# Kernel tuning notes

Hardware: AMD Instinct MI355X
Metric: run time of the kernel (lower is better)

## Reference

```python
import jax, jax.numpy as jnp
import numpy as np

# NF4 codebook (bitsandbytes values)
NF4_LEVELS = jnp.array([-1.0, -0.6961928009986877, -0.5250730514526367, -0.39491748809814453,
                        -0.28444138169288635, -0.18477343022823334, -0.09105003625154495, 0.0,
                        0.07958029955625534, 0.16093020141124725, 0.24611230194568634,
                        0.33791524171829224, 0.44070982933044434, 0.5626170039176941,
                        0.7229568362236023, 1.0], dtype=jnp.float32)

IN_FEATURES = 4096
OUT_FEATURES = 4096


def setup_inputs() -> dict:
    key = jax.random.key(0)
    k1, k2, k3, k4 = jax.random.split(key, 4)
    x = jax.random.normal(k1, (4, 2048, IN_FEATURES), dtype=jnp.float32)
    # packed uint8 bytes (stored as int32 in [0,256)), shape (O, I//2)
    packed = jax.random.randint(k2, (OUT_FEATURES, IN_FEATURES // 2), 0, 256, dtype=jnp.int32)
    absmax = jax.random.uniform(k3, (OUT_FEATURES,), dtype=jnp.float32) + 1e-3
    bias = jax.random.normal(k4, (OUT_FEATURES,), dtype=jnp.float32)
    return {"x": x, "packed": packed, "absmax": absmax, "bias": bias}


def dequantize_nf4(packed, absmax):
    # packed: (O, I//2) int bytes; high nibble first, then low nibble
    high = (packed >> 4) & 15
    low = packed & 15
    idx = jnp.stack([high, low], axis=2).reshape(packed.shape[0], -1)  # (O, I)
    w = NF4_LEVELS[idx]                    # LUT dequant, (O, I)
    return w * absmax[:, None]             # per-row absmax scaling


def reference(x, packed, absmax, bias):
    # forward: dequantize weight on-the-fly, then F.linear(x, W, bias)
    w = dequantize_nf4(packed, absmax)     # (O, I)
    return jnp.einsum('bsi,oi->bso', x, w) + bias
```

## Files before the change

### kernel.cpp

```cpp
#include <hip/hip_runtime.h>
#include <hip/hip_bf16.h>
#include <stdint.h>

#define M_DIM 8192
#define N_DIM 4096
#define K_DIM 4096

typedef __bf16 bf16_t;
typedef __attribute__((ext_vector_type(8))) __bf16 bf16x8;
typedef __attribute__((ext_vector_type(4))) float f32x4;

__constant__ float NF4_LUT[16] = {
    -1.0f, -0.6961928009986877f, -0.5250730514526367f, -0.39491748809814453f,
    -0.28444138169288635f, -0.18477343022823334f, -0.09105003625154495f, 0.0f,
    0.07958029955625534f, 0.16093020141124725f, 0.24611230194568634f,
    0.33791524171829224f, 0.44070982933044434f, 0.5626170039176941f,
    0.7229568362236023f, 1.0f};

__global__ __launch_bounds__(256) void dequant_nf4_kernel(
    const int* __restrict__ packed, const float* __restrict__ absmax,
    bf16_t* __restrict__ W) {
  const int t = blockIdx.x * 256 + threadIdx.x;
  const int row = t >> 9;
  const int c = t & 511;
  const int4 p = ((const int4*)packed)[t];
  const float am = absmax[row];
  bf16x8 v;
  int bytes0 = p.x & 255, bytes1 = p.y & 255, bytes2 = p.z & 255, bytes3 = p.w & 255;
  v[0] = (bf16_t)(NF4_LUT[(bytes0 >> 4) & 15] * am);
  v[1] = (bf16_t)(NF4_LUT[bytes0 & 15] * am);
  v[2] = (bf16_t)(NF4_LUT[(bytes1 >> 4) & 15] * am);
  v[3] = (bf16_t)(NF4_LUT[bytes1 & 15] * am);
  v[4] = (bf16_t)(NF4_LUT[(bytes2 >> 4) & 15] * am);
  v[5] = (bf16_t)(NF4_LUT[bytes2 & 15] * am);
  v[6] = (bf16_t)(NF4_LUT[(bytes3 >> 4) & 15] * am);
  v[7] = (bf16_t)(NF4_LUT[bytes3 & 15] * am);
  *((bf16x8*)&W[(size_t)row * K_DIM + c * 8]) = v;
}

__global__ __launch_bounds__(256) void cvt_bf16_kernel(
    const float* __restrict__ x, bf16_t* __restrict__ y) {
  const int t = blockIdx.x * 256 + threadIdx.x;
  const float4 a = ((const float4*)x)[2 * t];
  const float4 b = ((const float4*)x)[2 * t + 1];
  bf16x8 v;
  v[0] = (bf16_t)a.x; v[1] = (bf16_t)a.y; v[2] = (bf16_t)a.z; v[3] = (bf16_t)a.w;
  v[4] = (bf16_t)b.x; v[5] = (bf16_t)b.y; v[6] = (bf16_t)b.z; v[7] = (bf16_t)b.w;
  *((bf16x8*)&y[(size_t)t * 8]) = v;
}

#define GLD_LDS16(g, l)                                                     \
  __builtin_amdgcn_global_load_lds(                                        \
      (const __attribute__((address_space(1))) void*)(g),                   \
      (__attribute__((address_space(3))) void*)(l), 16, 0, 0)

__global__ __launch_bounds__(256) void gemm_nf4_kernel(
    const bf16_t* __restrict__ A, const bf16_t* __restrict__ B,
    const float* __restrict__ bias, float* __restrict__ C) {
  constexpr int BM = 128, BN = 128, BK = 32;
  __shared__ __align__(16) bf16_t sA[BM * BK];
  __shared__ __align__(16) bf16_t sB[BN * BK];

  const int tid = threadIdx.x;
  const int wave = tid >> 6, lane = tid & 63;
  const int wr = wave >> 1, wc = wave & 1;
  const int quad = lane >> 4, l15 = lane & 15;

  const int blockM = blockIdx.y * BM;
  const int blockN = blockIdx.x * BN;

  const int sr = tid >> 2;
  const int sk = (tid & 3) * 8;
  const bf16_t* gA0 = A + (size_t)(blockM + sr) * K_DIM + sk;
  const bf16_t* gA1 = gA0 + (size_t)64 * K_DIM;
  const bf16_t* gB0 = B + (size_t)(blockN + sr) * K_DIM + sk;
  const bf16_t* gB1 = gB0 + (size_t)64 * K_DIM;
  bf16_t* lA0 = &sA[tid * 8];
  bf16_t* lA1 = &sA[tid * 8 + 64 * BK];
  bf16_t* lB0 = &sB[tid * 8];
  bf16_t* lB1 = &sB[tid * 8 + 64 * BK];

  f32x4 acc[4][4];
#pragma unroll
  for (int i = 0; i < 4; ++i)
#pragma unroll
    for (int j = 0; j < 4; ++j) acc[i][j] = (f32x4)(0.0f);

  for (int k0 = 0; k0 < K_DIM; k0 += BK) {
    GLD_LDS16(gA0 + k0, lA0);
    GLD_LDS16(gA1 + k0, lA1);
    GLD_LDS16(gB0 + k0, lB0);
    GLD_LDS16(gB1 + k0, lB1);
    __syncthreads();

    bf16x8 af[4], bfr[4];
#pragma unroll
    for (int i = 0; i < 4; ++i)
      af[i] = *(const bf16x8*)&sA[(wr * 64 + i * 16 + l15) * BK + quad * 8];
#pragma unroll
    for (int j = 0; j < 4; ++j)
      bfr[j] = *(const bf16x8*)&sB[(wc * 64 + j * 16 + l15) * BK + quad * 8];

#pragma unroll
    for (int i = 0; i < 4; ++i)
#pragma unroll
      for (int j = 0; j < 4; ++j)
        acc[i][j] = __builtin_amdgcn_mfma_f32_16x16x32_bf16(af[i], bfr[j],
                                                            acc[i][j], 0, 0, 0);
    __syncthreads();
  }

#pragma unroll
  for (int j = 0; j < 4; ++j) {
    const int n = blockN + wc * 64 + j * 16 + l15;
    const float bv = bias[n];
#pragma unroll
    for (int i = 0; i < 4; ++i) {
      const int m0 = blockM + wr * 64 + i * 16 + quad * 4;
      f32x4 v = acc[i][j];
      C[(size_t)(m0 + 0) * N_DIM + n] = v[0] + bv;
      C[(size_t)(m0 + 1) * N_DIM + n] = v[1] + bv;
      C[(size_t)(m0 + 2) * N_DIM + n] = v[2] + bv;
      C[(size_t)(m0 + 3) * N_DIM + n] = v[3] + bv;
    }
  }
}

__global__ __launch_bounds__(256) void fallback_kernel(
    const float* __restrict__ x, const int* __restrict__ packed,
    const float* __restrict__ absmax, const float* __restrict__ bias,
    float* __restrict__ out) {
  const int idx = blockIdx.x * 256 + threadIdx.x;
  const int m = idx / N_DIM, n = idx % N_DIM;
  const int* prow = packed + (size_t)n * (K_DIM / 2);
  const float* xr = x + (size_t)m * K_DIM;
  float s = 0.0f;
  for (int p = 0; p < K_DIM / 2; ++p) {
    const int b = prow[p] & 255;
    s += xr[2 * p] * NF4_LUT[(b >> 4) & 15] + xr[2 * p + 1] * NF4_LUT[b & 15];
  }
  out[idx] = s * absmax[n] + bias[n];
}

extern "C" void kernel_launch(void* const* d_in, const int* in_sizes, int n_in,
                              void* d_out, int out_size, void* d_ws,
                              size_t ws_size, hipStream_t stream) {
  const float* x = (const float*)d_in[0];
  const int* packed = (const int*)d_in[1];
  const float* absmax = (const float*)d_in[2];
  const float* bias = (const float*)d_in[3];
  float* out = (float*)d_out;

  const size_t wBytes = (size_t)N_DIM * K_DIM * sizeof(bf16_t);
  const size_t xBytes = (size_t)M_DIM * K_DIM * sizeof(bf16_t);
  if (ws_size < wBytes + xBytes) {
    fallback_kernel<<<dim3((M_DIM * N_DIM) / 256), dim3(256), 0, stream>>>(
        x, packed, absmax, bias, out);
    return;
  }

  bf16_t* W = (bf16_t*)d_ws;
  bf16_t* xb = (bf16_t*)((char*)d_ws + wBytes);

  dequant_nf4_kernel<<<dim3((N_DIM * (K_DIM / 2) / 4) / 256), dim3(256), 0,
                       stream>>>(packed, absmax, W);
  cvt_bf16_kernel<<<dim3((M_DIM * K_DIM / 8) / 256), dim3(256), 0, stream>>>(
      x, xb);
  gemm_nf4_kernel<<<dim3(N_DIM / 128, M_DIM / 128), dim3(256), 0, stream>>>(
      xb, W, bias, out);
}
```

Measured before the change: 545.8 us.

## Use conflict-free LDS layout in GEMM, bpermute LUT dequant, narrower cvt

Changes the GEMM's LDS staging layout so each 16-row by 32-k fragment sits contiguously in lane order. Fragment reads then become linear per-lane 16-byte loads instead of row-strided loads that conflict on LDS banks. The dequant kernel replaces constant-memory LUT lookups with ds_bpermute against a per-lane copy of the LUT held in registers. The conversion kernel moves to 4 elements per thread with more blocks. The cvt change may reduce memory efficiency slightly because each thread now issues smaller stores.

Result: slower. 712.4 us (+30.5%).

```diff
diff --git a/kernel.cpp b/kernel.cpp
--- a/kernel.cpp
+++ b/kernel.cpp
@@ -8,6 +8,7 @@
 
 typedef __bf16 bf16_t;
 typedef __attribute__((ext_vector_type(8))) __bf16 bf16x8;
+typedef __attribute__((ext_vector_type(4))) __bf16 bf16x4;
 typedef __attribute__((ext_vector_type(4))) float f32x4;
 
 __constant__ float NF4_LUT[16] = {
@@ -23,30 +24,32 @@
   const int t = blockIdx.x * 256 + threadIdx.x;
   const int row = t >> 9;
   const int c = t & 511;
+  const int lane = threadIdx.x & 63;
+  const int lutbits = __float_as_int(NF4_LUT[lane & 15]);
+
   const int4 p = ((const int4*)packed)[t];
   const float am = absmax[row];
   bf16x8 v;
-  int bytes0 = p.x & 255, bytes1 = p.y & 255, bytes2 = p.z & 255, bytes3 = p.w & 255;
-  v[0] = (bf16_t)(NF4_LUT[(bytes0 >> 4) & 15] * am);
-  v[1] = (bf16_t)(NF4_LUT[bytes0 & 15] * am);
-  v[2] = (bf16_t)(NF4_LUT[(bytes1 >> 4) & 15] * am);
-  v[3] = (bf16_t)(NF4_LUT[bytes1 & 15] * am);
-  v[4] = (bf16_t)(NF4_LUT[(bytes2 >> 4) & 15] * am);
-  v[5] = (bf16_t)(NF4_LUT[bytes2 & 15] * am);
-  v[6] = (bf16_t)(NF4_LUT[(bytes3 >> 4) & 15] * am);
-  v[7] = (bf16_t)(NF4_LUT[bytes3 & 15] * am);
+#pragma unroll
+  for (int q = 0; q < 4; ++q) {
+    const int byte = (q == 0 ? p.x : q == 1 ? p.y : q == 2 ? p.z : p.w) & 255;
+    const float hi =
+        __int_as_float(__builtin_amdgcn_ds_bpermute(((byte >> 4) & 15) << 2, lutbits));
+    const float lo =
+        __int_as_float(__builtin_amdgcn_ds_bpermute((byte & 15) << 2, lutbits));
+    v[2 * q] = (bf16_t)(hi * am);
+    v[2 * q + 1] = (bf16_t)(lo * am);
+  }
   *((bf16x8*)&W[(size_t)row * K_DIM + c * 8]) = v;
 }
 
 __global__ __launch_bounds__(256) void cvt_bf16_kernel(
     const float* __restrict__ x, bf16_t* __restrict__ y) {
   const int t = blockIdx.x * 256 + threadIdx.x;
-  const float4 a = ((const float4*)x)[2 * t];
-  const float4 b = ((const float4*)x)[2 * t + 1];
-  bf16x8 v;
+  const float4 a = ((const float4*)x)[t];
+  bf16x4 v;
   v[0] = (bf16_t)a.x; v[1] = (bf16_t)a.y; v[2] = (bf16_t)a.z; v[3] = (bf16_t)a.w;
-  v[4] = (bf16_t)b.x; v[5] = (bf16_t)b.y; v[6] = (bf16_t)b.z; v[7] = (bf16_t)b.w;
-  *((bf16x8*)&y[(size_t)t * 8]) = v;
+  *((bf16x4*)&y[(size_t)t * 4]) = v;
 }
 
 #define GLD_LDS16(g, l)                                                     \
@@ -69,16 +72,16 @@
   const int blockM = blockIdx.y * BM;
   const int blockN = blockIdx.x * BN;
 
-  const int sr = tid >> 2;
-  const int sk = (tid & 3) * 8;
+  const int sr = ((tid >> 6) << 4) | (tid & 15);
+  const int sk = ((tid >> 4) & 3) * 8;
   const bf16_t* gA0 = A + (size_t)(blockM + sr) * K_DIM + sk;
   const bf16_t* gA1 = gA0 + (size_t)64 * K_DIM;
   const bf16_t* gB0 = B + (size_t)(blockN + sr) * K_DIM + sk;
   const bf16_t* gB1 = gB0 + (size_t)64 * K_DIM;
   bf16_t* lA0 = &sA[tid * 8];
-  bf16_t* lA1 = &sA[tid * 8 + 64 * BK];
+  bf16_t* lA1 = &sA[(tid + 256) * 8];
   bf16_t* lB0 = &sB[tid * 8];
-  bf16_t* lB1 = &sB[tid * 8 + 64 * BK];
+  bf16_t* lB1 = &sB[(tid + 256) * 8];
 
   f32x4 acc[4][4];
 #pragma unroll
@@ -96,10 +99,10 @@
     bf16x8 af[4], bfr[4];
 #pragma unroll
     for (int i = 0; i < 4; ++i)
-      af[i] = *(const bf16x8*)&sA[(wr * 64 + i * 16 + l15) * BK + quad * 8];
+      af[i] = *(const bf16x8*)&sA[((wr * 4 + i) * 64 + lane) * 8];
 #pragma unroll
     for (int j = 0; j < 4; ++j)
-      bfr[j] = *(const bf16x8*)&sB[(wc * 64 + j * 16 + l15) * BK + quad * 8];
+      bfr[j] = *(const bf16x8*)&sB[((wc * 4 + j) * 64 + lane) * 8];
 
 #pragma unroll
     for (int i = 0; i < 4; ++i)
@@ -164,7 +167,7 @@
 
   dequant_nf4_kernel<<<dim3((N_DIM * (K_DIM / 2) / 4) / 256), dim3(256), 0,
                        stream>>>(packed, absmax, W);
-  cvt_bf16_kernel<<<dim3((M_DIM * K_DIM / 8) / 256), dim3(256), 0, stream>>>(
+  cvt_bf16_kernel<<<dim3((M_DIM * K_DIM / 4) / 256), dim3(256), 0, stream>>>(
       x, xb);
   gemm_nf4_kernel<<<dim3(N_DIM / 128, M_DIM / 128), dim3(256), 0, stream>>>(
       xb, W, bias, out);
```
